# Optimization experiments

Hardware: AMD Instinct MI355X
Metric: run time of the kernel (lower is better)

The kernel has to match this reference:

```python
import jax, jax.numpy as jnp
import numpy as np

N, F, H, C = 4096, 512, 8, 128
LEAKY_ALPHA = 0.2
MASK_VAL = -10e9  # spektral uses -10e9 * (1 - A)


def setup_inputs() -> dict:
    key = jax.random.key(0)
    k1, k2, k3, k4, k5 = jax.random.split(key, 5)
    X = jax.random.normal(k1, (N, F), dtype=jnp.float32)
    # sparse-ish binary adjacency with self loops (dense layout as the layer expects)
    A = (jax.random.uniform(k2, (N, N)) < 0.01).astype(jnp.float32)
    A = jnp.maximum(A, jnp.eye(N, dtype=jnp.float32))
    W = jax.random.normal(k3, (H, F, C), dtype=jnp.float32) * (1.0 / np.sqrt(F))
    a_self = jax.random.normal(k4, (H, C), dtype=jnp.float32) * (1.0 / np.sqrt(C))
    a_neigh = jax.random.normal(k5, (H, C), dtype=jnp.float32) * (1.0 / np.sqrt(C))
    bias = jnp.zeros((H, C), dtype=jnp.float32)
    return {"X": X, "A": A, "W": W, "a_self": a_self, "a_neigh": a_neigh, "bias": bias}


def reference(X, A, W, a_self, a_neigh, bias):
    # per-head feature projection: [H, N, C]
    feats = jnp.einsum("nf,hfc->hnc", X, W)
    # attention scores e_ij = LeakyReLU(a_self . h_i + a_neigh . h_j)
    s_self = jnp.einsum("hnc,hc->hn", feats, a_self)    # [H, N]
    s_neigh = jnp.einsum("hnc,hc->hn", feats, a_neigh)  # [H, N]
    dense = s_self[:, :, None] + s_neigh[:, None, :]    # [H, N, N]
    dense = jnp.where(dense > 0, dense, LEAKY_ALPHA * dense)
    # adjacency mask then row softmax (dropout_rate=0 -> identity)
    dense = dense + MASK_VAL * (1.0 - A)[None, :, :]
    coef = jax.nn.softmax(dense, axis=-1)               # [H, N, N]
    out = jnp.einsum("hnm,hmc->hnc", coef, feats)       # [H, N, C]
    out = out + bias[:, None, :]
    # concat heads: [N, H*C]
    out = jnp.transpose(out, (1, 0, 2)).reshape(N, H * C)
    return jax.nn.relu(out)
```

## Files before the change

kernel.cpp:

```cpp
#include <hip/hip_runtime.h>
#include <hip/hip_bf16.h>

#define GN 4096
#define GF 512
#define GH 8
#define GC 128
#define CAP 256
#define BK 64
#define XS 72

typedef __hip_bfloat16 bf16;
typedef unsigned short u16;
typedef unsigned int u32;
typedef __attribute__((ext_vector_type(8))) short bf16x8;
typedef __attribute__((ext_vector_type(4))) float f32x4;

static __device__ inline u16 f2u16(float x) {
    union { bf16 b; u16 u; } cv;
    cv.b = __float2bfloat16(x);
    return cv.u;
}

__global__ __launch_bounds__(256) void feats_kernel(
    const float* __restrict__ X, const float* __restrict__ W,
    const float* __restrict__ a_self, const float* __restrict__ a_neigh,
    bf16* __restrict__ featsb, float* __restrict__ s_self,
    float* __restrict__ s_neigh)
{
    __shared__ u16 sX[64 * XS];
    __shared__ u16 sW[128 * XS];

    int h   = blockIdx.x >> 6;
    int n0  = (blockIdx.x & 63) << 6;
    int tid = threadIdx.x;
    int lane = tid & 63, wv = tid >> 6;
    int lm = lane & 15, q = lane >> 4;

    const float* Xp = X + (size_t)n0 * GF;
    const float* Wh = W + (size_t)h * GF * GC;

    f32x4 acc[8];
#pragma unroll
    for (int nt = 0; nt < 8; ++nt) acc[nt] = (f32x4){0.f, 0.f, 0.f, 0.f};

    for (int k0 = 0; k0 < GF; k0 += BK) {
        __syncthreads();
#pragma unroll
        for (int it = 0; it < 4; ++it) {
            int idx = it * 256 + tid;
            int row = idx >> 4, q4 = idx & 15;
            float4 v = *(const float4*)&Xp[(size_t)row * GF + k0 + q4 * 4];
            u16* d = &sX[row * XS + q4 * 4];
            d[0] = f2u16(v.x); d[1] = f2u16(v.y);
            d[2] = f2u16(v.z); d[3] = f2u16(v.w);
        }
#pragma unroll
        for (int it = 0; it < 8; ++it) {
            int idx = it * 256 + tid;
            int k = idx >> 5, n4 = idx & 31;
            float4 v = *(const float4*)&Wh[(size_t)(k0 + k) * GC + n4 * 4];
            sW[(n4 * 4 + 0) * XS + k] = f2u16(v.x);
            sW[(n4 * 4 + 1) * XS + k] = f2u16(v.y);
            sW[(n4 * 4 + 2) * XS + k] = f2u16(v.z);
            sW[(n4 * 4 + 3) * XS + k] = f2u16(v.w);
        }
        __syncthreads();

#pragma unroll
        for (int ks = 0; ks < BK; ks += 32) {
            bf16x8 af = *(const bf16x8*)&sX[(wv * 16 + lm) * XS + ks + q * 8];
            bf16x8 bfr[8];
#pragma unroll
            for (int nt = 0; nt < 8; ++nt)
                bfr[nt] = *(const bf16x8*)&sW[(nt * 16 + lm) * XS + ks + q * 8];
#pragma unroll
            for (int nt = 0; nt < 8; ++nt)
                acc[nt] = __builtin_amdgcn_mfma_f32_16x16x32_bf16(
                    af, bfr[nt], acc[nt], 0, 0, 0);
        }
    }

    float aS[8], aN[8];
#pragma unroll
    for (int nt = 0; nt < 8; ++nt) {
        aS[nt] = a_self[h * GC + nt * 16 + lm];
        aN[nt] = a_neigh[h * GC + nt * 16 + lm];
    }
    float vs[4] = {0.f, 0.f, 0.f, 0.f};
    float vn[4] = {0.f, 0.f, 0.f, 0.f};
    int rbase = n0 + wv * 16 + q * 4;
#pragma unroll
    for (int nt = 0; nt < 8; ++nt) {
        f32x4 v = acc[nt];
        int col = nt * 16 + lm;
#pragma unroll
        for (int r = 0; r < 4; ++r) {
            featsb[((size_t)h * GN + rbase + r) * GC + col] = __float2bfloat16(v[r]);
            vs[r] += v[r] * aS[nt];
            vn[r] += v[r] * aN[nt];
        }
    }
#pragma unroll
    for (int r = 0; r < 4; ++r) {
        for (int off = 1; off < 16; off <<= 1) {
            vs[r] += __shfl_xor(vs[r], off);
            vn[r] += __shfl_xor(vn[r], off);
        }
        if (lm == 0) {
            s_self[h * GN + rbase + r]  = vs[r];
            s_neigh[h * GN + rbase + r] = vn[r];
        }
    }
}

__global__ __launch_bounds__(256) void csr_kernel(
    const float* __restrict__ A, int* __restrict__ deg,
    u16* __restrict__ lists)
{
    int i    = blockIdx.x;
    int tid  = threadIdx.x;
    int lane = tid & 63;
    __shared__ int cnt;
    if (tid == 0) cnt = 0;
    __syncthreads();

    u16* row = lists + (size_t)i * CAP;
    const float4* Arow = (const float4*)(A + (size_t)i * GN);
    unsigned long long ltmask = (lane == 63) ? ~0ull >> 1
                                             : (1ull << lane) - 1;
#pragma unroll
    for (int it = 0; it < 4; ++it) {
        int qd = it * 256 + tid;
        float4 a = Arow[qd];
        int j = qd * 4;
#pragma unroll
        for (int comp = 0; comp < 4; ++comp) {
            float av = comp == 0 ? a.x : comp == 1 ? a.y : comp == 2 ? a.z : a.w;
            bool flag = av > 0.5f;
            unsigned long long m = __ballot(flag);
            if (m) {
                int base = 0;
                if (lane == 0) base = atomicAdd(&cnt, __popcll(m));
                base = __shfl(base, 0);
                if (flag) {
                    int s = base + __popcll(m & ltmask);
                    if (s < CAP) row[s] = (u16)(j + comp);
                }
            }
        }
    }
    __syncthreads();
    if (tid == 0) deg[i] = cnt < CAP ? cnt : CAP;
}

__global__ __launch_bounds__(128) void attn_kernel(
    const int* __restrict__ deg, const u16* __restrict__ lists,
    const float* __restrict__ bias, const bf16* __restrict__ featsb,
    const float* __restrict__ s_self, const float* __restrict__ s_neigh,
    float* __restrict__ out)
{
    int h   = blockIdx.x >> 12;
    int i   = blockIdx.x & (GN - 1);
    int tid = threadIdx.x;

    __shared__ float2 pj[CAP];
    __shared__ float  sacc[2][64][2];
    __shared__ float  redbuf[2];

    int M = deg[i];
    const u16* row = lists + (size_t)i * CAP;
    for (int k = tid; k < M; k += 128) pj[k].y = __int_as_float((int)row[k]);
    __syncthreads();

    float ssi = s_self[h * GN + i];
    const float* snh = s_neigh + h * GN;
    for (int k = tid; k < M; k += 128) {
        float e = ssi + snh[__float_as_int(pj[k].y)];
        pj[k].x = e > 0.f ? e : 0.2f * e;
    }
    __syncthreads();

    int lane = tid & 63, wv = tid >> 6;

    float m = -1e30f;
    for (int k = tid; k < M; k += 128) m = fmaxf(m, pj[k].x);
    for (int off = 32; off > 0; off >>= 1) m = fmaxf(m, __shfl_down(m, off));
    if (lane == 0) redbuf[wv] = m;
    __syncthreads();
    m = fmaxf(redbuf[0], redbuf[1]);
    __syncthreads();

    float s = 0.f;
    for (int k = tid; k < M; k += 128) {
        float e = __expf(pj[k].x - m);
        pj[k].x = e;
        s += e;
    }
    for (int off = 32; off > 0; off >>= 1) s += __shfl_down(s, off);
    __syncthreads();
    if (lane == 0) redbuf[wv] = s;
    __syncthreads();
    float inv = 1.f / (redbuf[0] + redbuf[1]);

    int c2 = tid & 63;
    const u32* fh = (const u32*)(featsb + (size_t)h * GN * GC) + c2;
    float acc0 = 0.f, acc1 = 0.f;
#pragma unroll 2
    for (int k = wv; k < M; k += 2) {
        float2 v = pj[k];
        int j = __float_as_int(v.y);
        u32 u = fh[(size_t)j << 6];
        float lo = __uint_as_float(u << 16);
        float hi = __uint_as_float(u & 0xffff0000u);
        acc0 += v.x * lo;
        acc1 += v.x * hi;
    }
    sacc[wv][c2][0] = acc0;
    sacc[wv][c2][1] = acc1;
    __syncthreads();

    if (tid < 64) {
        float r0 = (sacc[0][tid][0] + sacc[1][tid][0]) * inv + bias[h * GC + 2 * tid];
        float r1 = (sacc[0][tid][1] + sacc[1][tid][1]) * inv + bias[h * GC + 2 * tid + 1];
        float2* op = (float2*)&out[(size_t)i * (GH * GC) + h * GC + 2 * tid];
        *op = make_float2(fmaxf(r0, 0.f), fmaxf(r1, 0.f));
    }
}

extern "C" void kernel_launch(void* const* d_in, const int* in_sizes, int n_in,
                              void* d_out, int out_size, void* d_ws, size_t ws_size,
                              hipStream_t stream)
{
    const float* X       = (const float*)d_in[0];
    const float* A       = (const float*)d_in[1];
    const float* W       = (const float*)d_in[2];
    const float* a_self  = (const float*)d_in[3];
    const float* a_neigh = (const float*)d_in[4];
    const float* bias    = (const float*)d_in[5];
    float* out = (float*)d_out;

    bf16*  featsb  = (bf16*)d_ws;
    float* s_self  = (float*)(featsb + (size_t)GH * GN * GC);
    float* s_neigh = s_self + (size_t)GH * GN;
    int*   deg     = (int*)(s_neigh + (size_t)GH * GN);
    u16*   lists   = (u16*)(deg + GN);

    feats_kernel<<<GH * 64, 256, 0, stream>>>(X, W, a_self, a_neigh,
                                              featsb, s_self, s_neigh);
    csr_kernel<<<GN, 256, 0, stream>>>(A, deg, lists);
    attn_kernel<<<GH * GN, 128, 0, stream>>>(deg, lists, bias, featsb,
                                             s_self, s_neigh, out);
}
```

Before: 201.6 us.

## Map one wavefront per (head,row) in attention and prefetch GEMM tiles into registers

The attention kernel now gives each 64-lane wavefront one (head,row) pair, four per 256-thread block. This removes block-level __syncthreads and shared-memory reductions in favour of wave shuffles, and the score computation is fused with the max pass. The feature GEMM loads the next K-tile from global memory into registers while MFMAs run on the current tile, overlapping load latency with compute. Costs are more live registers in the GEMM and a serial neighbour loop per wave, which is longer per row since it is no longer split across two waves.

```diff
diff --git a/kernel.cpp b/kernel.cpp
--- a/kernel.cpp
+++ b/kernel.cpp
@@ -39,32 +39,51 @@
     const float* Xp = X + (size_t)n0 * GF;
     const float* Wh = W + (size_t)h * GF * GC;
 
+    int xrow = tid >> 4, xq4 = tid & 15;
+    int wk = tid >> 5, wn4 = tid & 31;
+
+    float4 xr[4], wr[8];
+
+#define ISSUE_TILE(K0)                                                        \
+    {                                                                         \
+        _Pragma("unroll")                                                     \
+        for (int it = 0; it < 4; ++it)                                        \
+            xr[it] = *(const float4*)&Xp[(size_t)(it * 16 + xrow) * GF +      \
+                                         (K0) + xq4 * 4];                     \
+        _Pragma("unroll")                                                     \
+        for (int it = 0; it < 8; ++it)                                        \
+            wr[it] = *(const float4*)&Wh[(size_t)((K0) + it * 8 + wk) * GC +  \
+                                         wn4 * 4];                            \
+    }
+
+#define STORE_TILE()                                                          \
+    {                                                                         \
+        _Pragma("unroll")                                                     \
+        for (int it = 0; it < 4; ++it) {                                      \
+            u16* d = &sX[(it * 16 + xrow) * XS + xq4 * 4];                    \
+            d[0] = f2u16(xr[it].x); d[1] = f2u16(xr[it].y);                   \
+            d[2] = f2u16(xr[it].z); d[3] = f2u16(xr[it].w);                   \
+        }                                                                     \
+        _Pragma("unroll")                                                     \
+        for (int it = 0; it < 8; ++it) {                                      \
+            int k = it * 8 + wk;                                              \
+            sW[(wn4 * 4 + 0) * XS + k] = f2u16(wr[it].x);                     \
+            sW[(wn4 * 4 + 1) * XS + k] = f2u16(wr[it].y);                     \
+            sW[(wn4 * 4 + 2) * XS + k] = f2u16(wr[it].z);                     \
+            sW[(wn4 * 4 + 3) * XS + k] = f2u16(wr[it].w);                     \
+        }                                                                     \
+    }
+
     f32x4 acc[8];
 #pragma unroll
     for (int nt = 0; nt < 8; ++nt) acc[nt] = (f32x4){0.f, 0.f, 0.f, 0.f};
+
+    ISSUE_TILE(0)
+    STORE_TILE()
 
     for (int k0 = 0; k0 < GF; k0 += BK) {
         __syncthreads();
-#pragma unroll
-        for (int it = 0; it < 4; ++it) {
-            int idx = it * 256 + tid;
-            int row = idx >> 4, q4 = idx & 15;
-            float4 v = *(const float4*)&Xp[(size_t)row * GF + k0 + q4 * 4];
-            u16* d = &sX[row * XS + q4 * 4];
-            d[0] = f2u16(v.x); d[1] = f2u16(v.y);
-            d[2] = f2u16(v.z); d[3] = f2u16(v.w);
-        }
-#pragma unroll
-        for (int it = 0; it < 8; ++it) {
-            int idx = it * 256 + tid;
-            int k = idx >> 5, n4 = idx & 31;
-            float4 v = *(const float4*)&Wh[(size_t)(k0 + k) * GC + n4 * 4];
-            sW[(n4 * 4 + 0) * XS + k] = f2u16(v.x);
-            sW[(n4 * 4 + 1) * XS + k] = f2u16(v.y);
-            sW[(n4 * 4 + 2) * XS + k] = f2u16(v.z);
-            sW[(n4 * 4 + 3) * XS + k] = f2u16(v.w);
-        }
-        __syncthreads();
+        if (k0 + BK < GF) ISSUE_TILE(k0 + BK)
 
 #pragma unroll
         for (int ks = 0; ks < BK; ks += 32) {
@@ -78,6 +97,8 @@
                 acc[nt] = __builtin_amdgcn_mfma_f32_16x16x32_bf16(
                     af, bfr[nt], acc[nt], 0, 0, 0);
         }
+        __syncthreads();
+        if (k0 + BK < GF) STORE_TILE()
     }
 
     float aS[8], aN[8];
@@ -111,6 +132,8 @@
             s_neigh[h * GN + rbase + r] = vn[r];
         }
     }
+#undef ISSUE_TILE
+#undef STORE_TILE
 }
 
 __global__ __launch_bounds__(256) void csr_kernel(
@@ -153,78 +176,64 @@
     if (tid == 0) deg[i] = cnt < CAP ? cnt : CAP;
 }
 
-__global__ __launch_bounds__(128) void attn_kernel(
+__global__ __launch_bounds__(256) void attn_kernel(
     const int* __restrict__ deg, const u16* __restrict__ lists,
     const float* __restrict__ bias, const bf16* __restrict__ featsb,
     const float* __restrict__ s_self, const float* __restrict__ s_neigh,
     float* __restrict__ out)
 {
-    int h   = blockIdx.x >> 12;
-    int i   = blockIdx.x & (GN - 1);
-    int tid = threadIdx.x;
-
-    __shared__ float2 pj[CAP];
-    __shared__ float  sacc[2][64][2];
-    __shared__ float  redbuf[2];
+    int tid  = threadIdx.x;
+    int wv   = tid >> 6, lane = tid & 63;
+    int g    = blockIdx.x * 4 + wv;
+    int h    = g >> 12;
+    int i    = g & (GN - 1);
+
+    __shared__ float2 pjbuf[4][CAP];
+    float2* pj = pjbuf[wv];
 
     int M = deg[i];
     const u16* row = lists + (size_t)i * CAP;
-    for (int k = tid; k < M; k += 128) pj[k].y = __int_as_float((int)row[k]);
-    __syncthreads();
-
     float ssi = s_self[h * GN + i];
     const float* snh = s_neigh + h * GN;
-    for (int k = tid; k < M; k += 128) {
-        float e = ssi + snh[__float_as_int(pj[k].y)];
-        pj[k].x = e > 0.f ? e : 0.2f * e;
-    }
-    __syncthreads();
-
-    int lane = tid & 63, wv = tid >> 6;
-
-    float m = -1e30f;
-    for (int k = tid; k < M; k += 128) m = fmaxf(m, pj[k].x);
-    for (int off = 32; off > 0; off >>= 1) m = fmaxf(m, __shfl_down(m, off));
-    if (lane == 0) redbuf[wv] = m;
-    __syncthreads();
-    m = fmaxf(redbuf[0], redbuf[1]);
-    __syncthreads();
-
-    float s = 0.f;
-    for (int k = tid; k < M; k += 128) {
-        float e = __expf(pj[k].x - m);
+
+    float lmax = -1e30f;
+    for (int k = lane; k < M; k += 64) {
+        int j = row[k];
+        float e = ssi + snh[j];
+        e = e > 0.f ? e : 0.2f * e;
+        pj[k] = make_float2(e, __int_as_float(j));
+        lmax = fmaxf(lmax, e);
+    }
+#pragma unroll
+    for (int off = 32; off > 0; off >>= 1)
+        lmax = fmaxf(lmax, __shfl_xor(lmax, off));
+
+    float lsum = 0.f;
+    for (int k = lane; k < M; k += 64) {
+        float e = __expf(pj[k].x - lmax);
         pj[k].x = e;
-        s += e;
-    }
-    for (int off = 32; off > 0; off >>= 1) s += __shfl_down(s, off);
-    __syncthreads();
-    if (lane == 0) redbuf[wv] = s;
-    __syncthreads();
-    float inv = 1.f / (redbuf[0] + redbuf[1]);
-
-    int c2 = tid & 63;
-    const u32* fh = (const u32*)(featsb + (size_t)h * GN * GC) + c2;
+        lsum += e;
+    }
+#pragma unroll
+    for (int off = 32; off > 0; off >>= 1) lsum += __shfl_xor(lsum, off);
+    float inv = 1.f / lsum;
+
+    const u32* fh = (const u32*)(featsb + (size_t)h * GN * GC) + lane;
     float acc0 = 0.f, acc1 = 0.f;
-#pragma unroll 2
-    for (int k = wv; k < M; k += 2) {
+#pragma unroll 4
+    for (int k = 0; k < M; ++k) {
         float2 v = pj[k];
         int j = __float_as_int(v.y);
         u32 u = fh[(size_t)j << 6];
-        float lo = __uint_as_float(u << 16);
-        float hi = __uint_as_float(u & 0xffff0000u);
-        acc0 += v.x * lo;
-        acc1 += v.x * hi;
-    }
-    sacc[wv][c2][0] = acc0;
-    sacc[wv][c2][1] = acc1;
-    __syncthreads();
-
-    if (tid < 64) {
-        float r0 = (sacc[0][tid][0] + sacc[1][tid][0]) * inv + bias[h * GC + 2 * tid];
-        float r1 = (sacc[0][tid][1] + sacc[1][tid][1]) * inv + bias[h * GC + 2 * tid + 1];
-        float2* op = (float2*)&out[(size_t)i * (GH * GC) + h * GC + 2 * tid];
-        *op = make_float2(fmaxf(r0, 0.f), fmaxf(r1, 0.f));
-    }
+        acc0 += v.x * __uint_as_float(u << 16);
+        acc1 += v.x * __uint_as_float(u & 0xffff0000u);
+    }
+
+    const float2 bv = *(const float2*)&bias[h * GC + 2 * lane];
+    float r0 = acc0 * inv + bv.x;
+    float r1 = acc1 * inv + bv.y;
+    float2* op = (float2*)&out[(size_t)i * (GH * GC) + h * GC + 2 * lane];
+    *op = make_float2(fmaxf(r0, 0.f), fmaxf(r1, 0.f));
 }
 
 extern "C" void kernel_launch(void* const* d_in, const int* in_sizes, int n_in,
@@ -248,6 +257,6 @@
     feats_kernel<<<GH * 64, 256, 0, stream>>>(X, W, a_self, a_neigh,
                                               featsb, s_self, s_neigh);
     csr_kernel<<<GN, 256, 0, stream>>>(A, deg, lists);
-    attn_kernel<<<GH * GN, 128, 0, stream>>>(deg, lists, bias, featsb,
-                                             s_self, s_neigh, out);
-}
+    attn_kernel<<<GH * GN / 4, 256, 0, stream>>>(deg, lists, bias, featsb,
+                                                 s_self, s_neigh, out);
+}
```

New measurement: 180.8 us. 10.3% less time.
